# Kernel tuning notes

Hardware: AMD Instinct MI355X
Metric: run time of the kernel (lower is better)

## Reference

```python
import jax, jax.numpy as jnp
import numpy as np

N = 50000      # nodes
E = 800000     # edges (avg degree 16)
IN = 64        # in_channels
OUT = 64       # out_channels
K = 3          # Chebyshev order
LAM = 2.0      # lambda_max for sym normalization


def setup_inputs() -> dict:
    key = jax.random.key(0)
    ks = jax.random.split(key, 16)
    s_in = 1.0 / np.sqrt(IN)
    s_out = 1.0 / np.sqrt(OUT)
    inp = {
        "X": jax.random.normal(ks[0], (N, IN), jnp.float32),
        "edge_index": jax.random.randint(ks[1], (2, E), 0, N, dtype=jnp.int64),
        "edge_weight": jax.random.uniform(ks[2], (E,), jnp.float32),
        # six ChebConv weight stacks [K, in, out] and biases [out]
        "W_xz": jax.random.normal(ks[3], (K, IN, OUT), jnp.float32) * s_in,
        "W_hz": jax.random.normal(ks[4], (K, OUT, OUT), jnp.float32) * s_out,
        "W_xr": jax.random.normal(ks[5], (K, IN, OUT), jnp.float32) * s_in,
        "W_hr": jax.random.normal(ks[6], (K, OUT, OUT), jnp.float32) * s_out,
        "W_xh": jax.random.normal(ks[7], (K, IN, OUT), jnp.float32) * s_in,
        "W_hh": jax.random.normal(ks[8], (K, OUT, OUT), jnp.float32) * s_out,
        "b_xz": jnp.zeros((OUT,), jnp.float32),
        "b_hz": jnp.zeros((OUT,), jnp.float32),
        "b_xr": jnp.zeros((OUT,), jnp.float32),
        "b_hr": jnp.zeros((OUT,), jnp.float32),
        "b_xh": jnp.zeros((OUT,), jnp.float32),
        "b_hh": jnp.zeros((OUT,), jnp.float32),
    }
    return inp


def _cheb_norm(edge_index, edge_weight):
    # PyG ChebConv __norm__ with sym normalization, lambda_max = 2:
    # L_hat = (2/lam) * (I - D^-1/2 A D^-1/2) - I
    src, dst = edge_index[0], edge_index[1]
    deg = jax.ops.segment_sum(edge_weight, src, num_segments=N)
    dinv = jnp.where(deg > 0, jax.lax.rsqrt(jnp.where(deg > 0, deg, 1.0)), 0.0)
    w_off = -(2.0 / LAM) * edge_weight * dinv[src] * dinv[dst]
    diag = 2.0 / LAM - 1.0  # 0 when lambda_max == 2
    return src, dst, w_off, diag


def _spmm(x, src, dst, w_off, diag):
    # y[i] = sum_{e: dst[e]=i} w_off[e] * x[src[e]] + diag * x[i]
    msg = w_off[:, None] * x[src]
    return jax.ops.segment_sum(msg, dst, num_segments=N) + diag * x


def _cheb_conv(x, W, b, src, dst, w_off, diag):
    Tx0 = x
    out = Tx0 @ W[0]
    Tx1 = _spmm(Tx0, src, dst, w_off, diag)
    out = out + Tx1 @ W[1]
    for k in range(2, K):
        Tx2 = 2.0 * _spmm(Tx1, src, dst, w_off, diag) - Tx0
        out = out + Tx2 @ W[k]
        Tx0, Tx1 = Tx1, Tx2
    return out + b


def reference(X, edge_index, edge_weight,
              W_xz, W_hz, W_xr, W_hr, W_xh, W_hh,
              b_xz, b_hz, b_xr, b_hr, b_xh, b_hh):
    src, dst, w_off, diag = _cheb_norm(edge_index, edge_weight)
    cheb = lambda x, W, b: _cheb_conv(x, W, b, src, dst, w_off, diag)
    H = jnp.zeros((N, OUT), X.dtype)  # _set_hidden_state with H=None
    Z = jax.nn.sigmoid(cheb(X, W_xz, b_xz) + cheb(H, W_hz, b_hz))
    R = jax.nn.sigmoid(cheb(X, W_xr, b_xr) + cheb(H, W_hr, b_hr))
    H_tilde = jnp.tanh(cheb(X, W_xh, b_xh) + cheb(H * R, W_hh, b_hh))
    H_new = Z * H + (1.0 - Z) * H_tilde
    return H_new
```

## Files before the change

kernel.cpp:

```cpp
#include <hip/hip_runtime.h>


#define N_NODES 50000
#define E_EDGES 800000
#define NC 64
#define BSH 6
#define BUKN 64
#define NBUK 782
#define EPB 2048
#define NBLK 391

#define OFF_CV       0
#define OFF_ROWSTART 1600000
#define OFF_TOTD     1650016
#define OFF_BASED    1650800
#define OFF_TOTS     1651584
#define OFF_BASES    1652368
#define OFF_TX1      1653152
#define OFF_RECD     1653152
#define OFF_DINV     3253152
#define OFF_CNTD     3303168
#define OFF_TX2      4853152
#define OFF_RECS     4853152
#define OFF_CNTS     6453152
#define OFF_WB       8053152

typedef __attribute__((ext_vector_type(8))) short bf16x8;
typedef __attribute__((ext_vector_type(4))) float f32x4;

__device__ __forceinline__ unsigned bf16rne(float x) {
    unsigned u = __float_as_uint(x);
    return (u + 0x7fffu + ((u >> 16) & 1u)) >> 16;
}

__global__ __launch_bounds__(256) void k_hist(const int* __restrict__ ei,
        int* __restrict__ cntD, int* __restrict__ cntS,
        const float* __restrict__ Wz, const float* __restrict__ Wh,
        short* __restrict__ WB) {
    int t = threadIdx.x, blk = blockIdx.x;
    if (blk >= NBLK) {
        int mg = blk - NBLK;
        int m = mg >> 1, g = mg & 1;
        const float* W = (g ? Wh : Wz) + m * 4096;
        #pragma unroll
        for (int r = 0; r < 16; ++r) {
            int idx = r * 256 + t;
            int c = idx >> 6, o = idx & 63;
            float x = W[idx];
            unsigned hi = bf16rne(x);
            float fhi = __uint_as_float(hi << 16);
            unsigned lo = bf16rne(x - fhi);
            WB[(mg * 2 + 0) * 4096 + o * 64 + c] = (short)hi;
            WB[(mg * 2 + 1) * 4096 + o * 64 + c] = (short)lo;
        }
        return;
    }
    __shared__ int hD[NBUK], hS[NBUK];
    for (int b = t; b < NBUK; b += 256) { hD[b] = 0; hS[b] = 0; }
    __syncthreads();
    int e0 = blk * EPB;
    #pragma unroll
    for (int i = 0; i < 8; ++i) {
        int e = e0 + i * 256 + t;
        if (e < E_EDGES) {
            atomicAdd(&hS[ei[e] >> BSH], 1);
            atomicAdd(&hD[ei[E_EDGES + e] >> BSH], 1);
        }
    }
    __syncthreads();
    for (int b = t; b < NBUK; b += 256) {
        cntD[b * NBLK + blk] = hD[b];
        cntS[b * NBLK + blk] = hS[b];
    }
}

__global__ __launch_bounds__(256) void k_scanPB(int* __restrict__ cntD,
        int* __restrict__ cntS, int* __restrict__ totD, int* __restrict__ totS) {
    __shared__ int s[512];
    int t = threadIdx.x;
    int row = blockIdx.x; int* cnt; int* tot;
    if (row < NBUK) { cnt = cntD; tot = totD; }
    else            { row -= NBUK; cnt = cntS; tot = totS; }
    int v0 = (t < NBLK) ? cnt[row * NBLK + t] : 0;
    int v1 = (256 + t < NBLK) ? cnt[row * NBLK + 256 + t] : 0;
    s[t] = v0; s[256 + t] = v1;
    __syncthreads();
    for (int off = 1; off < 512; off <<= 1) {
        int a = (t >= off) ? s[t - off] : 0;
        int b = (256 + t >= off) ? s[256 + t - off] : 0;
        __syncthreads();
        s[t] += a; s[256 + t] += b;
        __syncthreads();
    }
    if (t < NBLK) cnt[row * NBLK + t] = s[t] - v0;
    if (256 + t < NBLK) cnt[row * NBLK + 256 + t] = s[256 + t] - v1;
    if (t == 0) tot[row] = s[511];
}

__global__ __launch_bounds__(256) void k_scanTot(int* __restrict__ totD,
        int* __restrict__ baseD, int* __restrict__ totS, int* __restrict__ baseS) {
    __shared__ int s[1024];
    int t = threadIdx.x;
    int* tot  = blockIdx.x ? totS  : totD;
    int* base = blockIdx.x ? baseS : baseD;
    int v[4];
    #pragma unroll
    for (int q = 0; q < 4; ++q) {
        int i = q * 256 + t;
        v[q] = (i < NBUK) ? tot[i] : 0;
        s[i] = v[q];
    }
    __syncthreads();
    for (int off = 1; off < 1024; off <<= 1) {
        int a[4];
        #pragma unroll
        for (int q = 0; q < 4; ++q) {
            int i = q * 256 + t;
            a[q] = (i >= off) ? s[i - off] : 0;
        }
        __syncthreads();
        #pragma unroll
        for (int q = 0; q < 4; ++q) s[q * 256 + t] += a[q];
        __syncthreads();
    }
    #pragma unroll
    for (int q = 0; q < 4; ++q) {
        int i = q * 256 + t;
        if (i < NBUK) base[i] = s[i] - v[q];
    }
}

__global__ __launch_bounds__(256) void k_scatter(const int* __restrict__ ei,
        const float* __restrict__ ew, const int* __restrict__ offD,
        const int* __restrict__ offS, const int* __restrict__ baseD,
        const int* __restrict__ baseS, long long* __restrict__ recD,
        long long* __restrict__ recS) {
    __shared__ int curD[NBUK], curS[NBUK];
    int t = threadIdx.x, blk = blockIdx.x;
    for (int b = t; b < NBUK; b += 256) {
        curD[b] = baseD[b] + offD[b * NBLK + blk];
        curS[b] = baseS[b] + offS[b * NBLK + blk];
    }
    __syncthreads();
    int e0 = blk * EPB;
    #pragma unroll
    for (int i = 0; i < 8; ++i) {
        int e = e0 + i * 256 + t;
        if (e < E_EDGES) {
            int sN = ei[e], dN = ei[E_EDGES + e];
            long long wb = (long long)(unsigned)__float_as_uint(ew[e]) << 32;
            int pD = atomicAdd(&curD[dN >> BSH], 1);
            recD[pD] = wb | (unsigned)((sN << BSH) | (dN & (BUKN - 1)));
            int pS = atomicAdd(&curS[sN >> BSH], 1);
            recS[pS] = wb | (unsigned)(sN & (BUKN - 1));
        }
    }
}

__global__ __launch_bounds__(256) void k_deg(const long long* __restrict__ recS,
        const int* __restrict__ totS, const int* __restrict__ baseS,
        float* __restrict__ dinv) {
    __shared__ float degL[BUKN];
    int t = threadIdx.x, b = blockIdx.x;
    if (t < BUKN) degL[t] = 0.f;
    __syncthreads();
    int st = baseS[b], n = totS[b];
    for (int i = t; i < n; i += 256) {
        long long r = recS[st + i];
        atomicAdd(&degL[(int)(r & (BUKN - 1))], __uint_as_float((unsigned)(r >> 32)));
    }
    __syncthreads();
    if (t < BUKN) {
        int node = b * BUKN + t;
        if (node < N_NODES) {
            float dg = degL[t];
            dinv[node] = dg > 0.f ? rsqrtf(dg) : 0.f;
        }
    }
}

__global__ __launch_bounds__(256) void k_csr(const long long* __restrict__ recD,
        const int* __restrict__ totD, const int* __restrict__ baseD,
        const float* __restrict__ dinv, long long* __restrict__ cv,
        int* __restrict__ row_start) {
    __shared__ int cnt[BUKN], cur[BUKN];
    __shared__ float dL[BUKN];
    int t = threadIdx.x, b = blockIdx.x;
    if (t < BUKN) {
        cnt[t] = 0;
        int node = b * BUKN + t;
        dL[t] = (node < N_NODES) ? dinv[node] : 0.f;
    }
    __syncthreads();
    int st = baseD[b], n = totD[b];
    for (int i = t; i < n; i += 256)
        atomicAdd(&cnt[(int)(recD[st + i] & (BUKN - 1))], 1);
    __syncthreads();
    if (t < BUKN) {
        int x = cnt[t];
        int orig = x;
        #pragma unroll
        for (int off = 1; off < BUKN; off <<= 1) {
            int v = __shfl_up(x, off, 64);
            if ((t & 63) >= off) x += v;
        }
        cur[t] = x - orig;
        int node = b * BUKN + t;
        if (node < N_NODES) row_start[node] = st + (x - orig);
    }
    if (b == 0 && t == 0) row_start[N_NODES] = E_EDGES;
    __syncthreads();
    for (int i = t; i < n; i += 256) {
        long long r = recD[st + i];
        int m = (int)(r & 0xffffffffLL);
        float w = __uint_as_float((unsigned)(r >> 32));
        int rr = m & (BUKN - 1);
        int sN = m >> BSH;
        float val = -w * dinv[sN] * dL[rr];
        int pos = st + atomicAdd(&cur[rr], 1);
        cv[pos] = ((long long)__float_as_int(val) << 32) | (unsigned)sN;
    }
}

template<int SCALE, int SUB>
__global__ __launch_bounds__(256) void k_spmm(
        const int* __restrict__ row_start, const long long* __restrict__ cv,
        const float* __restrict__ xin, const float* __restrict__ xprev,
        float* __restrict__ out) {
    int wid = (blockIdx.x << 2) + (threadIdx.x >> 6);
    int l = threadIdx.x & 63;
    if (wid >= N_NODES) return;
    int start = row_start[wid];
    int end   = row_start[wid + 1];
    int sub = l >> 4;
    int q   = l & 15;
    float4 acc = make_float4(0.f, 0.f, 0.f, 0.f);
    for (int j = start; j < end; j += 8) {
        int jA = j + sub;
        int jB = j + 4 + sub;
        long long pA = (jA < end) ? cv[jA] : 0LL;
        long long pB = (jB < end) ? cv[jB] : 0LL;
        float4 xA = *(const float4*)&xin[(size_t)(unsigned)(pA & 0xffffffffLL) * NC + q * 4];
        float4 xB = *(const float4*)&xin[(size_t)(unsigned)(pB & 0xffffffffLL) * NC + q * 4];
        float vA = __int_as_float((int)(pA >> 32));
        float vB = __int_as_float((int)(pB >> 32));
        acc.x = fmaf(vA, xA.x, acc.x);
        acc.y = fmaf(vA, xA.y, acc.y);
        acc.z = fmaf(vA, xA.z, acc.z);
        acc.w = fmaf(vA, xA.w, acc.w);
        acc.x = fmaf(vB, xB.x, acc.x);
        acc.y = fmaf(vB, xB.y, acc.y);
        acc.z = fmaf(vB, xB.z, acc.z);
        acc.w = fmaf(vB, xB.w, acc.w);
    }
    #pragma unroll
    for (int m = 16; m <= 32; m <<= 1) {
        acc.x += __shfl_xor(acc.x, m, 64);
        acc.y += __shfl_xor(acc.y, m, 64);
        acc.z += __shfl_xor(acc.z, m, 64);
        acc.w += __shfl_xor(acc.w, m, 64);
    }
    if (sub == 0) {
        float4 r;
        r.x = (float)SCALE * acc.x;
        r.y = (float)SCALE * acc.y;
        r.z = (float)SCALE * acc.z;
        r.w = (float)SCALE * acc.w;
        if (SUB) {
            float4 xo = *(const float4*)&xprev[(size_t)wid * NC + q * 4];
            r.x -= xo.x; r.y -= xo.y; r.z -= xo.z; r.w -= xo.w;
        }
        *(float4*)&out[(size_t)wid * NC + q * 4] = r;
    }
}

__global__ __launch_bounds__(256) void k_gru(
        const float* __restrict__ X, const float* __restrict__ Tx1,
        const float* __restrict__ Tx2, const short* __restrict__ WB,
        const float* __restrict__ bxz, const float* __restrict__ bhz,
        const float* __restrict__ bxh, const float* __restrict__ bhh,
        float* __restrict__ out) {
    __shared__ short Ahi[64 * 64];
    __shared__ short Alo[64 * 64];
    int tid = threadIdx.x;
    int l = tid & 63;
    int w = tid >> 6;
    int node0 = blockIdx.x * 64;

    f32x4 accz[4], acch[4];
    #pragma unroll
    for (int mt = 0; mt < 4; ++mt) {
        accz[mt] = (f32x4){0.f, 0.f, 0.f, 0.f};
        acch[mt] = (f32x4){0.f, 0.f, 0.f, 0.f};
    }

    const float* ins[3] = {X, Tx1, Tx2};
    #pragma unroll 1
    for (int m = 0; m < 3; ++m) {
        __syncthreads();
        const float* ip = ins[m];
        #pragma unroll
        for (int r = 0; r < 4; ++r) {
            int fidx = r * 256 + tid;
            int n = fidx >> 4, c4 = fidx & 15;
            int gn = node0 + n;
            float4 v = make_float4(0.f, 0.f, 0.f, 0.f);
            if (gn < N_NODES) v = *(const float4*)&ip[(size_t)gn * 64 + c4 * 4];
            unsigned h0 = bf16rne(v.x), h1 = bf16rne(v.y),
                     h2 = bf16rne(v.z), h3 = bf16rne(v.w);
            unsigned q0 = bf16rne(v.x - __uint_as_float(h0 << 16));
            unsigned q1 = bf16rne(v.y - __uint_as_float(h1 << 16));
            unsigned q2 = bf16rne(v.z - __uint_as_float(h2 << 16));
            unsigned q3 = bf16rne(v.w - __uint_as_float(h3 << 16));
            int kk = (c4 * 4) ^ ((n & 7) << 3);
            *(uint2*)&Ahi[n * 64 + kk] = make_uint2(h0 | (h1 << 16), h2 | (h3 << 16));
            *(uint2*)&Alo[n * 64 + kk] = make_uint2(q0 | (q1 << 16), q2 | (q3 << 16));
        }
        __syncthreads();
        const short* wbm = WB + m * 4 * 4096;
        #pragma unroll
        for (int kt = 0; kt < 2; ++kt) {
            int k0 = kt * 32 + (l >> 4) * 8;
            bf16x8 ah[4], al[4];
            #pragma unroll
            for (int mt = 0; mt < 4; ++mt) {
                int row = mt * 16 + (l & 15);
                int kk = k0 ^ ((row & 7) << 3);
                ah[mt] = *(const bf16x8*)&Ahi[row * 64 + kk];
                al[mt] = *(const bf16x8*)&Alo[row * 64 + kk];
            }
            int o = w * 16 + (l & 15);
            {
                bf16x8 bh_ = *(const bf16x8*)&wbm[0 * 4096 + o * 64 + k0];
                bf16x8 bl_ = *(const bf16x8*)&wbm[1 * 4096 + o * 64 + k0];
                #pragma unroll
                for (int mt = 0; mt < 4; ++mt) {
                    accz[mt] = __builtin_amdgcn_mfma_f32_16x16x32_bf16(ah[mt], bh_, accz[mt], 0, 0, 0);
                    accz[mt] = __builtin_amdgcn_mfma_f32_16x16x32_bf16(ah[mt], bl_, accz[mt], 0, 0, 0);
                    accz[mt] = __builtin_amdgcn_mfma_f32_16x16x32_bf16(al[mt], bh_, accz[mt], 0, 0, 0);
                }
            }
            {
                bf16x8 bh_ = *(const bf16x8*)&wbm[2 * 4096 + o * 64 + k0];
                bf16x8 bl_ = *(const bf16x8*)&wbm[3 * 4096 + o * 64 + k0];
                #pragma unroll
                for (int mt = 0; mt < 4; ++mt) {
                    acch[mt] = __builtin_amdgcn_mfma_f32_16x16x32_bf16(ah[mt], bh_, acch[mt], 0, 0, 0);
                    acch[mt] = __builtin_amdgcn_mfma_f32_16x16x32_bf16(ah[mt], bl_, acch[mt], 0, 0, 0);
                    acch[mt] = __builtin_amdgcn_mfma_f32_16x16x32_bf16(al[mt], bh_, acch[mt], 0, 0, 0);
                }
            }
        }
    }

    int o = w * 16 + (l & 15);
    float bz = bxz[o] + bhz[o];
    float bh = bxh[o] + bhh[o];
    #pragma unroll
    for (int mt = 0; mt < 4; ++mt) {
        #pragma unroll
        for (int r = 0; r < 4; ++r) {
            int node = node0 + mt * 16 + (l >> 4) * 4 + r;
            if (node < N_NODES) {
                float z = accz[mt][r] + bz;
                float h = acch[mt][r] + bh;
                float sig = 1.f / (1.f + __expf(-z));
                float e2 = __expf(-2.f * h);
                float th = (1.f - e2) / (1.f + e2);
                out[(size_t)node * 64 + o] = (1.f - sig) * th;
            }
        }
    }
}

extern "C" void kernel_launch(void* const* d_in, const int* in_sizes, int n_in,
                              void* d_out, int out_size, void* d_ws, size_t ws_size,
                              hipStream_t stream) {
    const float* X   = (const float*)d_in[0];
    const int*   ei  = (const int*)d_in[1];
    const float* ew  = (const float*)d_in[2];
    const float* Wxz = (const float*)d_in[3];
    const float* Wxh = (const float*)d_in[7];
    const float* bxz = (const float*)d_in[9];
    const float* bhz = (const float*)d_in[10];
    const float* bxh = (const float*)d_in[13];
    const float* bhh = (const float*)d_in[14];
    float* out = (float*)d_out;

    float* ws_f = (float*)d_ws;
    int*   ws_i = (int*)d_ws;

    long long* cv       = (long long*)(ws_i + OFF_CV);
    int*       rowstart = ws_i + OFF_ROWSTART;
    int*       totD     = ws_i + OFF_TOTD;
    int*       baseD    = ws_i + OFF_BASED;
    int*       totS     = ws_i + OFF_TOTS;
    int*       baseS    = ws_i + OFF_BASES;
    float*     tx1      = ws_f + OFF_TX1;
    long long* recD     = (long long*)(ws_i + OFF_RECD);
    float*     dinv     = ws_f + OFF_DINV;
    int*       cntD     = ws_i + OFF_CNTD;
    float*     tx2      = ws_f + OFF_TX2;
    long long* recS     = (long long*)(ws_i + OFF_RECS);
    int*       cntS     = ws_i + OFF_CNTS;
    short*     WB       = (short*)(ws_i + OFF_WB);

    const int TB = 256;
    k_hist<<<NBLK + 6, TB, 0, stream>>>(ei, cntD, cntS, Wxz, Wxh, WB);
    k_scanPB<<<2 * NBUK, TB, 0, stream>>>(cntD, cntS, totD, totS);
    k_scanTot<<<2, TB, 0, stream>>>(totD, baseD, totS, baseS);
    k_scatter<<<NBLK, TB, 0, stream>>>(ei, ew, cntD, cntS, baseD, baseS, recD, recS);
    k_deg<<<NBUK, TB, 0, stream>>>(recS, totS, baseS, dinv);
    k_csr<<<NBUK, TB, 0, stream>>>(recD, totD, baseD, dinv, cv, rowstart);

    k_spmm<1, 0><<<(N_NODES + 3) / 4, TB, 0, stream>>>(rowstart, cv, X, X, tx1);
    k_spmm<2, 1><<<(N_NODES + 3) / 4, TB, 0, stream>>>(rowstart, cv, tx1, X, tx2);

    k_gru<<<NBUK, TB, 0, stream>>>(X, tx1, tx2, WB, bxz, bhz, bxh, bhh, out);
}
```

Before: 147.1 us.

## Fuse degree and CSR kernels, pre-scale source features by dinv

Merges the degree and CSR-build kernels into one launch. The source-side D^-1/2 factor moves out of the per-edge value and into prescaled feature buffers (xs = dinv*X, and u1 = dinv*Tx1 written by the first SpMM pass). This drops the random dinv[src] gather during CSR construction. The cost is extra writes of two N×64 buffers, plus a larger workspace layout that no longer aliases recD/recS with tx1/tx2.

```diff
diff --git a/kernel.cpp b/kernel.cpp
--- a/kernel.cpp
+++ b/kernel.cpp
@@ -16,14 +16,16 @@
 #define OFF_BASED    1650800
 #define OFF_TOTS     1651584
 #define OFF_BASES    1652368
-#define OFF_TX1      1653152
-#define OFF_RECD     1653152
-#define OFF_DINV     3253152
-#define OFF_CNTD     3303168
-#define OFF_TX2      4853152
-#define OFF_RECS     4853152
-#define OFF_CNTS     6453152
-#define OFF_WB       8053152
+#define OFF_CNTD     1653152
+#define OFF_CNTS     1958914
+#define OFF_DINV     2264676
+#define OFF_WB       2314724
+#define OFF_RECD     2339300
+#define OFF_RECS     3939300
+#define OFF_XS       5539300
+#define OFF_TX1      8739300
+#define OFF_U1       11939300
+#define OFF_TX2      15139300
 
 typedef __attribute__((ext_vector_type(8))) short bf16x8;
 typedef __attribute__((ext_vector_type(4))) float f32x4;
@@ -157,44 +159,47 @@
     }
 }
 
-__global__ __launch_bounds__(256) void k_deg(const long long* __restrict__ recS,
-        const int* __restrict__ totS, const int* __restrict__ baseS,
-        float* __restrict__ dinv) {
-    __shared__ float degL[BUKN];
+__global__ __launch_bounds__(256) void k_degcsr(
+        const long long* __restrict__ recS, const int* __restrict__ totS,
+        const int* __restrict__ baseS, const long long* __restrict__ recD,
+        const int* __restrict__ totD, const int* __restrict__ baseD,
+        const float* __restrict__ X, float* __restrict__ dinv,
+        float* __restrict__ xs, long long* __restrict__ cv,
+        int* __restrict__ row_start) {
+    __shared__ float degL[BUKN], dinvL[BUKN];
+    __shared__ int cnt[BUKN], cur[BUKN];
     int t = threadIdx.x, b = blockIdx.x;
-    if (t < BUKN) degL[t] = 0.f;
-    __syncthreads();
-    int st = baseS[b], n = totS[b];
-    for (int i = t; i < n; i += 256) {
-        long long r = recS[st + i];
+    if (t < BUKN) { degL[t] = 0.f; cnt[t] = 0; }
+    __syncthreads();
+    int stS = baseS[b], nS = totS[b];
+    for (int i = t; i < nS; i += 256) {
+        long long r = recS[stS + i];
         atomicAdd(&degL[(int)(r & (BUKN - 1))], __uint_as_float((unsigned)(r >> 32)));
     }
     __syncthreads();
     if (t < BUKN) {
         int node = b * BUKN + t;
-        if (node < N_NODES) {
-            float dg = degL[t];
-            dinv[node] = dg > 0.f ? rsqrtf(dg) : 0.f;
-        }
-    }
-}
-
-__global__ __launch_bounds__(256) void k_csr(const long long* __restrict__ recD,
-        const int* __restrict__ totD, const int* __restrict__ baseD,
-        const float* __restrict__ dinv, long long* __restrict__ cv,
-        int* __restrict__ row_start) {
-    __shared__ int cnt[BUKN], cur[BUKN];
-    __shared__ float dL[BUKN];
-    int t = threadIdx.x, b = blockIdx.x;
-    if (t < BUKN) {
-        cnt[t] = 0;
-        int node = b * BUKN + t;
-        dL[t] = (node < N_NODES) ? dinv[node] : 0.f;
-    }
-    __syncthreads();
-    int st = baseD[b], n = totD[b];
-    for (int i = t; i < n; i += 256)
-        atomicAdd(&cnt[(int)(recD[st + i] & (BUKN - 1))], 1);
+        float dg = degL[t];
+        float dv = (node < N_NODES && dg > 0.f) ? rsqrtf(dg) : 0.f;
+        dinvL[t] = dv;
+        if (node < N_NODES) dinv[node] = dv;
+    }
+    __syncthreads();
+    #pragma unroll
+    for (int it = 0; it < 4; ++it) {
+        int fidx = it * 256 + t;
+        int n = fidx >> 4, c4 = fidx & 15;
+        int gn = b * BUKN + n;
+        if (gn < N_NODES) {
+            float4 v = *(const float4*)&X[(size_t)gn * 64 + c4 * 4];
+            float dv = dinvL[n];
+            float4 sv = make_float4(dv * v.x, dv * v.y, dv * v.z, dv * v.w);
+            *(float4*)&xs[(size_t)gn * 64 + c4 * 4] = sv;
+        }
+    }
+    int stD = baseD[b], nD = totD[b];
+    for (int i = t; i < nD; i += 256)
+        atomicAdd(&cnt[(int)(recD[stD + i] & (BUKN - 1))], 1);
     __syncthreads();
     if (t < BUKN) {
         int x = cnt[t];
@@ -206,27 +211,28 @@
         }
         cur[t] = x - orig;
         int node = b * BUKN + t;
-        if (node < N_NODES) row_start[node] = st + (x - orig);
+        if (node < N_NODES) row_start[node] = stD + (x - orig);
     }
     if (b == 0 && t == 0) row_start[N_NODES] = E_EDGES;
     __syncthreads();
-    for (int i = t; i < n; i += 256) {
-        long long r = recD[st + i];
+    for (int i = t; i < nD; i += 256) {
+        long long r = recD[stD + i];
         int m = (int)(r & 0xffffffffLL);
         float w = __uint_as_float((unsigned)(r >> 32));
         int rr = m & (BUKN - 1);
         int sN = m >> BSH;
-        float val = -w * dinv[sN] * dL[rr];
-        int pos = st + atomicAdd(&cur[rr], 1);
+        float val = -w * dinvL[rr];
+        int pos = stD + atomicAdd(&cur[rr], 1);
         cv[pos] = ((long long)__float_as_int(val) << 32) | (unsigned)sN;
     }
 }
 
-template<int SCALE, int SUB>
+template<int PASS>
 __global__ __launch_bounds__(256) void k_spmm(
         const int* __restrict__ row_start, const long long* __restrict__ cv,
-        const float* __restrict__ xin, const float* __restrict__ xprev,
-        float* __restrict__ out) {
+        const float* __restrict__ gsrc, const float* __restrict__ X,
+        const float* __restrict__ dinv, float* __restrict__ out1,
+        float* __restrict__ out2) {
     int wid = (blockIdx.x << 2) + (threadIdx.x >> 6);
     int l = threadIdx.x & 63;
     if (wid >= N_NODES) return;
@@ -240,8 +246,8 @@
         int jB = j + 4 + sub;
         long long pA = (jA < end) ? cv[jA] : 0LL;
         long long pB = (jB < end) ? cv[jB] : 0LL;
-        float4 xA = *(const float4*)&xin[(size_t)(unsigned)(pA & 0xffffffffLL) * NC + q * 4];
-        float4 xB = *(const float4*)&xin[(size_t)(unsigned)(pB & 0xffffffffLL) * NC + q * 4];
+        float4 xA = *(const float4*)&gsrc[(size_t)(unsigned)(pA & 0xffffffffLL) * NC + q * 4];
+        float4 xB = *(const float4*)&gsrc[(size_t)(unsigned)(pB & 0xffffffffLL) * NC + q * 4];
         float vA = __int_as_float((int)(pA >> 32));
         float vB = __int_as_float((int)(pB >> 32));
         acc.x = fmaf(vA, xA.x, acc.x);
@@ -261,16 +267,17 @@
         acc.w += __shfl_xor(acc.w, m, 64);
     }
     if (sub == 0) {
-        float4 r;
-        r.x = (float)SCALE * acc.x;
-        r.y = (float)SCALE * acc.y;
-        r.z = (float)SCALE * acc.z;
-        r.w = (float)SCALE * acc.w;
-        if (SUB) {
-            float4 xo = *(const float4*)&xprev[(size_t)wid * NC + q * 4];
-            r.x -= xo.x; r.y -= xo.y; r.z -= xo.z; r.w -= xo.w;
-        }
-        *(float4*)&out[(size_t)wid * NC + q * 4] = r;
+        if (PASS == 1) {
+            *(float4*)&out1[(size_t)wid * NC + q * 4] = acc;
+            float dv = dinv[wid];
+            float4 u = make_float4(dv * acc.x, dv * acc.y, dv * acc.z, dv * acc.w);
+            *(float4*)&out2[(size_t)wid * NC + q * 4] = u;
+        } else {
+            float4 xo = *(const float4*)&X[(size_t)wid * NC + q * 4];
+            float4 r = make_float4(2.f * acc.x - xo.x, 2.f * acc.y - xo.y,
+                                   2.f * acc.z - xo.z, 2.f * acc.w - xo.w);
+            *(float4*)&out1[(size_t)wid * NC + q * 4] = r;
+        }
     }
 }
 
@@ -396,25 +403,27 @@
     int*       baseD    = ws_i + OFF_BASED;
     int*       totS     = ws_i + OFF_TOTS;
     int*       baseS    = ws_i + OFF_BASES;
+    int*       cntD     = ws_i + OFF_CNTD;
+    int*       cntS     = ws_i + OFF_CNTS;
+    float*     dinv     = ws_f + OFF_DINV;
+    short*     WB       = (short*)(ws_i + OFF_WB);
+    long long* recD     = (long long*)(ws_i + OFF_RECD);
+    long long* recS     = (long long*)(ws_i + OFF_RECS);
+    float*     xs       = ws_f + OFF_XS;
     float*     tx1      = ws_f + OFF_TX1;
-    long long* recD     = (long long*)(ws_i + OFF_RECD);
-    float*     dinv     = ws_f + OFF_DINV;
-    int*       cntD     = ws_i + OFF_CNTD;
+    float*     u1       = ws_f + OFF_U1;
     float*     tx2      = ws_f + OFF_TX2;
-    long long* recS     = (long long*)(ws_i + OFF_RECS);
-    int*       cntS     = ws_i + OFF_CNTS;
-    short*     WB       = (short*)(ws_i + OFF_WB);
 
     const int TB = 256;
     k_hist<<<NBLK + 6, TB, 0, stream>>>(ei, cntD, cntS, Wxz, Wxh, WB);
     k_scanPB<<<2 * NBUK, TB, 0, stream>>>(cntD, cntS, totD, totS);
     k_scanTot<<<2, TB, 0, stream>>>(totD, baseD, totS, baseS);
     k_scatter<<<NBLK, TB, 0, stream>>>(ei, ew, cntD, cntS, baseD, baseS, recD, recS);
-    k_deg<<<NBUK, TB, 0, stream>>>(recS, totS, baseS, dinv);
-    k_csr<<<NBUK, TB, 0, stream>>>(recD, totD, baseD, dinv, cv, rowstart);
-
-    k_spmm<1, 0><<<(N_NODES + 3) / 4, TB, 0, stream>>>(rowstart, cv, X, X, tx1);
-    k_spmm<2, 1><<<(N_NODES + 3) / 4, TB, 0, stream>>>(rowstart, cv, tx1, X, tx2);
+    k_degcsr<<<NBUK, TB, 0, stream>>>(recS, totS, baseS, recD, totD, baseD,
+                                      X, dinv, xs, cv, rowstart);
+
+    k_spmm<1><<<(N_NODES + 3) / 4, TB, 0, stream>>>(rowstart, cv, xs, X, dinv, tx1, u1);
+    k_spmm<2><<<(N_NODES + 3) / 4, TB, 0, stream>>>(rowstart, cv, u1, X, dinv, tx2, u1);
 
     k_gru<<<NBUK, TB, 0, stream>>>(X, tx1, tx2, WB, bxz, bhz, bxh, bhh, out);
 }
```

Measured after the change: 162.1 us. +10.2%, slower.
